# Performance work log

Measured on AMD Instinct MI355X. Metric: run time of the kernel, lower is better.

Reference implementation:

```python
import jax, jax.numpy as jnp
import numpy as np

EPS = 1e-8
B, T, D = 2, 512, 64
L = 4        # n_layers
NPASS = 2    # n_recursive_passes


def setup_inputs() -> dict:
    key = jax.random.key(0)
    ks = jax.random.split(key, 8)
    H = D // 2
    r = lambda k, shape, s=0.05: jax.random.normal(k, shape, dtype=jnp.float32) * s
    return {
        "basin_seq": jax.random.normal(ks[0], (B, T, D), dtype=jnp.float32),
        "basin_coords": r(ks[1], (D,), 0.1),
        "W_temp": r(ks[2], (L, 1, D)),
        "b_temp": jnp.zeros((L, 1), jnp.float32),
        "res_scale": jnp.full((L,), 0.1, jnp.float32),
        "W_fb": r(ks[3], (L, D, 2 * D)),
        "b_fb": jnp.zeros((L, D), jnp.float32),
        "Wc1": r(ks[4], (H, D)),
        "bc1": jnp.zeros((H,), jnp.float32),
        "Wc2": r(ks[5], (D, H)),
        "bc2": jnp.zeros((D,), jnp.float32),
        "Wu": r(ks[6], (D, 2 * D)),
        "bu": jnp.zeros((D,), jnp.float32),
        "res_scale_g": jnp.asarray(1.0, jnp.float32),
    }


def _project_to_simplex(x):
    s = jax.nn.softplus(x)
    s = s / (s.sum(axis=-1, keepdims=True) + EPS)
    return jnp.maximum(s, EPS)


def _qfi_attention_weights(x, temperature):
    # x: (B,T,D); temperature: scalar
    p = _project_to_simplex(x)
    # fisher_rao_distance_simplex renormalizes its inputs again
    p = p / (p.sum(axis=-1, keepdims=True) + EPS)
    # pairwise Bhattacharyya-like inner product: (B,T,T,D) broadcast -> (B,T,T)
    inner = jnp.sqrt(p[:, :, None, :] * p[:, None, :, :] + EPS).sum(axis=-1)
    inner = jnp.clip(inner, -1.0 + 1e-6, 1.0 - 1e-6)
    d = 2.0 * jnp.arccos(inner)                      # Fisher-Rao distance (B,T,T)
    logits = -d / jnp.maximum(temperature, 1e-6)
    return jax.nn.softmax(logits, axis=-1)


def _forward(basin_seq, basin_coords, W_temp, b_temp, res_scale, W_fb, b_fb,
             Wc1, bc1, Wc2, bc2, Wu, bu, res_scale_g):
    x = basin_seq
    current_basin = basin_coords                     # (D,)
    layer_states = [[None] * L for _ in range(NPASS)]
    for p_idx in range(NPASS):
        for l in range(L):
            prev = layer_states[p_idx - 1][l] if p_idx > 0 else None
            if prev is not None:
                combined = jnp.concatenate([x, prev], axis=-1)          # (B,T,2D)
                gate = jax.nn.sigmoid(combined @ W_fb[l].T + b_fb[l])   # (B,T,D)
                x = x * gate + prev * (1.0 - gate)
            # BasinCoupledQFIAttention (dropout inactive in eval)
            tm = jax.nn.sigmoid(W_temp[l] @ current_basin + b_temp[l]) + 0.5
            temperature = jax.lax.stop_gradient(tm.mean())  # torch uses .item()
            w = _qfi_attention_weights(x, temperature)
            x_attn = jnp.einsum('bij,bjd->bid', w, x)
            x = x + res_scale[l] * (x_attn - x)
            layer_states[p_idx][l] = x
        # holographic encode: mean-pool then compress MLP (tanh, tanh)
        pooled = x.mean(axis=1)                                         # (B,D)
        hidden_basin = jnp.tanh(jnp.tanh(pooled @ Wc1.T + bc1) @ Wc2.T + bc2)
        if p_idx < NPASS - 1:
            aggregated = hidden_basin.mean(axis=0)                      # (D,)
            comb = jnp.concatenate([current_basin, aggregated], axis=-1)
            g = jax.nn.sigmoid(Wu @ comb + bu)
            current_basin = current_basin * (1.0 - g) + aggregated * g
    output = x + 0.01 * res_scale_g * (x - basin_seq)
    return output


def reference(basin_seq, basin_coords, W_temp, b_temp, res_scale, W_fb, b_fb,
              Wc1, bc1, Wc2, bc2, Wu, bu, res_scale_g):
    return _forward(basin_seq, basin_coords, W_temp, b_temp, res_scale, W_fb,
                    b_fb, Wc1, bc1, Wc2, bc2, Wu, bu, res_scale_g)
```

## Files before the change

kernel.cpp:

```cpp
#include <hip/hip_runtime.h>
#include <math.h>

#define EPSF 1e-8f
#define Tn 512
#define Dn 64
#define NELEM 65536

typedef _Float16 half_t;
typedef __attribute__((ext_vector_type(4))) _Float16 half4;

__device__ __forceinline__ float sigmoidf_(float x){ return 1.0f/(1.0f+expf(-x)); }
__device__ __forceinline__ float softplusf_(float x){ return fmaxf(x,0.0f) + log1pf(expf(-fabsf(x))); }

__device__ __forceinline__ float wrs(float v){
  #pragma unroll
  for (int off=1; off<64; off<<=1) v += __shfl_xor(v, off, 64);
  return v;
}
__device__ __forceinline__ float wrm(float v){
  #pragma unroll
  for (int off=1; off<64; off<<=1) v = fmaxf(v, __shfl_xor(v, off, 64));
  return v;
}

__device__ __forceinline__ void pnorm_w(float xg, int b, int r, int row, int d,
                                        float* __restrict__ sbuf_out,
                                        half_t* __restrict__ sTh_out){
  float s = softplusf_(xg);
  float sum = wrs(s);
  float p = fmaxf(s/(sum+EPSF), EPSF);
  float s2 = wrs(p);
  float sq = sqrtf(p/(s2+EPSF));
  sbuf_out[(size_t)row*Dn + d] = sq;
  sTh_out[(size_t)b*Dn*Tn + (size_t)d*Tn + r] = (half_t)sq;
}

__global__ __launch_bounds__(256) void k_prologue(
    const float* __restrict__ basin_seq, float* __restrict__ sA, half_t* __restrict__ sThA,
    half_t* __restrict__ xhBS,
    const float* __restrict__ W_temp, const float* __restrict__ b_temp,
    const float* __restrict__ cb0, float* __restrict__ temps){
  int tid = threadIdx.x, wid = tid>>6, lane = tid&63;
  if (blockIdx.x < 256){
    int row = blockIdx.x*4 + wid;
    float xv = basin_seq[(size_t)row*Dn+lane];
    xhBS[(size_t)row*Dn+lane] = (half_t)xv;
    pnorm_w(xv, row>>9, row&511, row, lane, sA, sThA);
  } else if (tid < 64){
    float cbv = cb0[tid];
    #pragma unroll
    for (int l=0;l<4;l++){
      float v = wrs(W_temp[l*Dn + tid]*cbv);
      if (tid==0) temps[l] = sigmoidf_(v + b_temp[l]) + 0.5f;
    }
  }
}

__device__ __forceinline__ void gate_dot2(float (*comb)[128], float* gred,
                                          const float* __restrict__ Wfb, int tid, int lane){
  int dd = tid >> 3, k8 = tid & 7;
  const float4* wp = (const float4*)(Wfb + (size_t)dd*128 + k8*16);
  float4 w0 = wp[0], w1 = wp[1], w2 = wp[2], w3 = wp[3];
  float ga[2];
  #pragma unroll
  for (int i=0;i<2;i++){
    float4 c0 = *(const float4*)&comb[i][k8*16];
    float4 c1 = *(const float4*)&comb[i][k8*16+4];
    float4 c2 = *(const float4*)&comb[i][k8*16+8];
    float4 c3 = *(const float4*)&comb[i][k8*16+12];
    ga[i] = w0.x*c0.x + w0.y*c0.y + w0.z*c0.z + w0.w*c0.w
          + w1.x*c1.x + w1.y*c1.y + w1.z*c1.z + w1.w*c1.w
          + w2.x*c2.x + w2.y*c2.y + w2.z*c2.z + w2.w*c2.w
          + w3.x*c3.x + w3.y*c3.y + w3.z*c3.z + w3.w*c3.w;
  }
  #pragma unroll
  for (int off=1; off<8; off<<=1){
    ga[0] += __shfl_xor(ga[0],off,64); ga[1] += __shfl_xor(ga[1],off,64);
  }
  if ((lane&7)==0){ gred[dd*3+0]=ga[0]; gred[dd*3+1]=ga[1]; }
}

template<int MODE>
__global__ __launch_bounds__(512) void k_attn(
    const float* __restrict__ xin, const half_t* __restrict__ xh,
    const float* __restrict__ sbuf, const half_t* __restrict__ sTh,
    const float* __restrict__ temps, const float* __restrict__ res_scale, int l,
    float* __restrict__ xout, float* __restrict__ xg_out, half_t* __restrict__ xh_out,
    float* __restrict__ sbuf_out, half_t* __restrict__ sTh_out,
    const float* __restrict__ Wfb, const float* __restrict__ bfb,
    const float* __restrict__ prev,
    const float* __restrict__ basin_seq, const float* __restrict__ rsg,
    float* __restrict__ pooled_g, const float* __restrict__ basin_coords,
    const float* __restrict__ Wc1, const float* __restrict__ bc1,
    const float* __restrict__ Wc2, const float* __restrict__ bc2,
    const float* __restrict__ Wu,  const float* __restrict__ bu,
    const float* __restrict__ W_temp, const float* __restrict__ b_temp){
  __shared__ __align__(16) union {
    float part[8*512];
    float pvp[32*2*64];
  } u;
  __shared__ __align__(8) float P[512*2];
  __shared__ __align__(8) float s_i[64*2];
  __shared__ float redw[2][8][2];
  __shared__ __align__(16) float comb[2][128];
  __shared__ float gred[64*3];
  __shared__ float pl[128], h1b[64], hbb[128], combb[128];
  __shared__ float tl_sh;

  int tid = threadIdx.x, wav = tid>>6, lane = tid&63;
  int row0 = blockIdx.x*2, b = row0>>9, r0 = row0&511;
  int i_ = tid>>6, d_ = lane;

  float xi_pre = 0.f, prev_pre = 0.f;
  if (tid < 128){
    s_i[d_*2 + i_] = sbuf[(size_t)(row0+i_)*Dn + d_];
    xi_pre = xin[(size_t)(row0+i_)*Dn + d_];
    if constexpr (MODE == 4 || MODE == 5) prev_pre = prev[(size_t)(row0+i_)*Dn + d_];
  }

  if constexpr (MODE == 5 || MODE == 6){
    if (tid < 128) pl[tid] = pooled_g[tid] * (1.0f/512.0f);
    __syncthreads();
    if (tid < 64){
      int bb=tid>>5, h=tid&31;
      float acc=0.f;
      #pragma unroll 8
      for (int d2=0; d2<64; d2++) acc += pl[bb*64+d2]*Wc1[h*64+d2];
      h1b[tid] = tanhf(acc + bc1[h]);
    }
    __syncthreads();
    if (tid < 128){
      int bb=tid>>6, dd=tid&63;
      float acc=0.f;
      #pragma unroll 8
      for (int h2=0; h2<32; h2++) acc += h1b[bb*32+h2]*Wc2[dd*32+h2];
      hbb[tid] = tanhf(acc + bc2[dd]);
    }
    __syncthreads();
    if (tid < 64){
      float agg = 0.5f*(hbb[tid] + hbb[64+tid]);
      combb[tid] = basin_coords[tid];
      combb[64+tid] = agg;
    }
    __syncthreads();
    if (tid < 64){
      float acc=0.f;
      #pragma unroll 8
      for (int k=0;k<128;k++) acc += Wu[tid*128+k]*combb[k];
      float g = sigmoidf_(acc + bu[tid]);
      float cbl = combb[tid]*(1.0f-g) + combb[64+tid]*g;
      float v = wrs(W_temp[l*Dn + tid]*cbl);
      if (tid==0) tl_sh = sigmoidf_(v + b_temp[l]) + 0.5f;
    }
  }
  __syncthreads();

  {
    int g = tid & 127, kq = tid >> 7;
    const half4* sT4 = (const half4*)(sTh + (size_t)b*Dn*Tn);
    float4 a0 = {0,0,0,0}, a1 = a0;
    int kb = kq*16;
    #pragma unroll
    for (int kk=0; kk<16; ++kk){
      int k = kb + kk;
      half4 vh = sT4[(size_t)k*128 + g];
      float vx=(float)vh.x, vy=(float)vh.y, vz=(float)vh.z, vw=(float)vh.w;
      float2 si = *(const float2*)&s_i[k*2];
      a0.x=fmaf(si.x,vx,a0.x); a0.y=fmaf(si.x,vy,a0.y);
      a0.z=fmaf(si.x,vz,a0.z); a0.w=fmaf(si.x,vw,a0.w);
      a1.x=fmaf(si.y,vx,a1.x); a1.y=fmaf(si.y,vy,a1.y);
      a1.z=fmaf(si.y,vz,a1.z); a1.w=fmaf(si.y,vw,a1.w);
    }
    *(float4*)&u.part[(0*4+kq)*512 + g*4] = a0;
    *(float4*)&u.part[(1*4+kq)*512 + g*4] = a1;
  }
  __syncthreads();
  {
    float invT;
    if constexpr (MODE == 5 || MODE == 6) invT = 1.0f/fmaxf(tl_sh, 1e-6f);
    else invT = 1.0f/fmaxf(temps[l], 1e-6f);
    int j = tid;
    float a0 = u.part[0*512+j] + u.part[1*512+j] + u.part[2*512+j] + u.part[3*512+j];
    float a1 = u.part[4*512+j] + u.part[5*512+j] + u.part[6*512+j] + u.part[7*512+j];
    float l0 = -2.0f*acosf(fminf(fmaxf(a0,-1.0f+1e-6f),1.0f-1e-6f))*invT;
    float l1 = -2.0f*acosf(fminf(fmaxf(a1,-1.0f+1e-6f),1.0f-1e-6f))*invT;
    float m0=wrm(l0), m1=wrm(l1);
    if (lane==0){ redw[0][wav][0]=m0; redw[0][wav][1]=m1; }
    __syncthreads();
    float mv0=redw[0][0][0], mv1=redw[0][0][1];
    #pragma unroll
    for (int w=1;w<8;w++){ mv0=fmaxf(mv0,redw[0][w][0]); mv1=fmaxf(mv1,redw[0][w][1]); }
    float e0=expf(l0-mv0), e1=expf(l1-mv1);
    float2 ev = {e0,e1};
    *(float2*)&P[j*2] = ev;
    float q0=wrs(e0), q1=wrs(e1);
    if (lane==0){ redw[1][wav][0]=q0; redw[1][wav][1]=q1; }
  }
  __syncthreads();
  {
    int jg = tid>>4, dq = tid&15;
    const half4* x4 = (const half4*)(xh + (size_t)b*Tn*Dn);
    float4 o0={0,0,0,0}, o1=o0;
    int jb = jg*16;
    #pragma unroll
    for (int jj=0; jj<16; ++jj){
      int j = jb + jj;
      half4 xvh = x4[(size_t)j*16 + dq];
      float xx=(float)xvh.x, xy=(float)xvh.y, xz=(float)xvh.z, xw=(float)xvh.w;
      float2 pw = *(const float2*)&P[j*2];
      o0.x=fmaf(pw.x,xx,o0.x); o0.y=fmaf(pw.x,xy,o0.y);
      o0.z=fmaf(pw.x,xz,o0.z); o0.w=fmaf(pw.x,xw,o0.w);
      o1.x=fmaf(pw.y,xx,o1.x); o1.y=fmaf(pw.y,xy,o1.y);
      o1.z=fmaf(pw.y,xz,o1.z); o1.w=fmaf(pw.y,xw,o1.w);
    }
    *(float4*)&u.pvp[(jg*2+0)*64 + dq*4] = o0;
    *(float4*)&u.pvp[(jg*2+1)*64 + dq*4] = o1;
  }
  __syncthreads();
  float o = 0.f;
  if (tid < 128){
    float ss = 0.f;
    #pragma unroll
    for (int jg=0; jg<32; ++jg) ss += u.pvp[(jg*2+i_)*64+d_];
    float sv = 0.f;
    #pragma unroll
    for (int w=0;w<8;w++) sv += redw[1][w][i_];
    float attn = ss/sv;
    o = xi_pre + res_scale[l]*(attn - xi_pre);
  }
  if constexpr (MODE == 0){
    if (tid < 128){
      xout[(size_t)(row0+i_)*Dn + d_] = o;
      xh_out[(size_t)(row0+i_)*Dn + d_] = (half_t)o;
      pnorm_w(o, b, r0+i_, row0+i_, d_, sbuf_out, sTh_out);
    }
  } else if constexpr (MODE == 4){
    if (tid < 128){
      xout[(size_t)(row0+i_)*Dn + d_] = o;
      atomicAdd(&pooled_g[b*64+d_], o);
      comb[i_][d_] = o;
      comb[i_][64+d_] = prev_pre;
    }
    __syncthreads();
    gate_dot2(comb, gred, Wfb, tid, lane);
    __syncthreads();
    if (tid < 128){
      float g = sigmoidf_(gred[d_*3+i_] + bfb[d_]);
      float xg = o*g + prev_pre*(1.0f-g);
      xg_out[(size_t)(row0+i_)*Dn + d_] = xg;
      xh_out[(size_t)(row0+i_)*Dn + d_] = (half_t)xg;
      pnorm_w(xg, b, r0+i_, row0+i_, d_, sbuf_out, sTh_out);
    }
  } else if constexpr (MODE == 5){
    if (tid < 128){
      comb[i_][d_] = o;
      comb[i_][64+d_] = prev_pre;
    }
    __syncthreads();
    gate_dot2(comb, gred, Wfb, tid, lane);
    __syncthreads();
    if (tid < 128){
      float g = sigmoidf_(gred[d_*3+i_] + bfb[d_]);
      float xg = o*g + prev_pre*(1.0f-g);
      xout[(size_t)(row0+i_)*Dn + d_] = xg;
      xh_out[(size_t)(row0+i_)*Dn + d_] = (half_t)xg;
      pnorm_w(xg, b, r0+i_, row0+i_, d_, sbuf_out, sTh_out);
    }
  } else {
    if (tid < 128){
      float c = 0.01f * rsg[0];
      xout[(size_t)(row0+i_)*Dn + d_] = o + c*(o - basin_seq[(size_t)(row0+i_)*Dn + d_]);
    }
  }
}

extern "C" void kernel_launch(void* const* d_in, const int* in_sizes, int n_in,
                              void* d_out, int out_size, void* d_ws, size_t ws_size,
                              hipStream_t stream) {
  const float* basin_seq    = (const float*)d_in[0];
  const float* basin_coords = (const float*)d_in[1];
  const float* W_temp       = (const float*)d_in[2];
  const float* b_temp       = (const float*)d_in[3];
  const float* res_scale    = (const float*)d_in[4];
  const float* W_fb         = (const float*)d_in[5];
  const float* b_fb         = (const float*)d_in[6];
  const float* Wc1          = (const float*)d_in[7];
  const float* bc1          = (const float*)d_in[8];
  const float* Wc2          = (const float*)d_in[9];
  const float* bc2          = (const float*)d_in[10];
  const float* Wu           = (const float*)d_in[11];
  const float* bu           = (const float*)d_in[12];
  const float* rsg          = (const float*)d_in[13];
  float* out = (float*)d_out;
  float* ws  = (float*)d_ws;

  const size_t N = NELEM;
  float* pooled_g = ws;
  float* temps    = ws + 192;
  float* base     = ws + 256;
  float* sA    = base;
  float* sB    = base + N;
  float* st0   = base + 2*N;
  float* st1   = base + 3*N;
  float* st2   = base + 4*N;
  float* st3   = base + 5*N;
  float* xA    = base + 6*N;
  float* xB    = base + 7*N;
  half_t* sThA = (half_t*)(base + 8*N);
  half_t* sThB = (half_t*)(base + 8*N + N/2);
  half_t* xhBS = (half_t*)(base + 9*N);
  half_t* xhA  = (half_t*)(base + 9*N + N/2);
  half_t* xhB  = (half_t*)(base + 10*N);

  const int GA = 512;

  (void)hipMemsetAsync(d_ws, 0, 1024, stream);

  k_prologue<<<257,256,0,stream>>>(basin_seq, sA, sThA, xhBS, W_temp, b_temp, basin_coords, temps);
  k_attn<0><<<GA,512,0,stream>>>(basin_seq, xhBS, sA, sThA, temps, res_scale, 0,
                                 st0, nullptr, xhA, sB, sThB,
                                 nullptr,nullptr,nullptr,nullptr,nullptr,
                                 nullptr,nullptr,nullptr,nullptr,nullptr,nullptr,nullptr,nullptr,nullptr,nullptr);
  k_attn<0><<<GA,512,0,stream>>>(st0, xhA, sB, sThB, temps, res_scale, 1,
                                 st1, nullptr, xhB, sA, sThA,
                                 nullptr,nullptr,nullptr,nullptr,nullptr,
                                 nullptr,nullptr,nullptr,nullptr,nullptr,nullptr,nullptr,nullptr,nullptr,nullptr);
  k_attn<0><<<GA,512,0,stream>>>(st1, xhB, sA, sThA, temps, res_scale, 2,
                                 st2, nullptr, xhA, sB, sThB,
                                 nullptr,nullptr,nullptr,nullptr,nullptr,
                                 nullptr,nullptr,nullptr,nullptr,nullptr,nullptr,nullptr,nullptr,nullptr,nullptr);
  k_attn<4><<<GA,512,0,stream>>>(st2, xhA, sB, sThB, temps, res_scale, 3,
                                 st3, xA, xhBS, sA, sThA,
                                 W_fb, b_fb, st0, nullptr,nullptr,
                                 pooled_g,nullptr,nullptr,nullptr,nullptr,nullptr,nullptr,nullptr,nullptr,nullptr);
  k_attn<5><<<GA,512,0,stream>>>(xA, xhBS, sA, sThA, nullptr, res_scale, 0,
                                 xB, nullptr, xhA, sB, sThB,
                                 W_fb + (size_t)1*Dn*2*Dn, b_fb + 1*Dn, st1, nullptr,nullptr,
                                 pooled_g, basin_coords, Wc1, bc1, Wc2, bc2, Wu, bu, W_temp, b_temp);
  k_attn<5><<<GA,512,0,stream>>>(xB, xhA, sB, sThB, nullptr, res_scale, 1,
                                 xA, nullptr, xhB, sA, sThA,
                                 W_fb + (size_t)2*Dn*2*Dn, b_fb + 2*Dn, st2, nullptr,nullptr,
                                 pooled_g, basin_coords, Wc1, bc1, Wc2, bc2, Wu, bu, W_temp, b_temp);
  k_attn<5><<<GA,512,0,stream>>>(xA, xhB, sA, sThA, nullptr, res_scale, 2,
                                 xB, nullptr, xhA, sB, sThB,
                                 W_fb + (size_t)3*Dn*2*Dn, b_fb + 3*Dn, st3, nullptr,nullptr,
                                 pooled_g, basin_coords, Wc1, bc1, Wc2, bc2, Wu, bu, W_temp, b_temp);
  k_attn<6><<<GA,512,0,stream>>>(xB, xhA, sB, sThB, nullptr, res_scale, 3,
                                 out, nullptr, nullptr, nullptr, nullptr,
                                 nullptr,nullptr,nullptr, basin_seq, rsg,
                                 pooled_g, basin_coords, Wc1, bc1, Wc2, bc2, Wu, bu, W_temp, b_temp);
}
```

Baseline: 199.1 us.

## Compute pass-two temperatures once in last block via atomic counter

Before, every block of the four second-pass attention kernels recomputed the compress MLP, the basin update and the temperature from pooled_g, each step separated by block barriers. Now the last block to finish the MODE 4 kernel, found through a threadfence and an atomic counter, computes all four second-pass temperatures once and writes them to a workspace array. Later kernels just read temps[l]. This removes redundant serial prologue work from four launches per block, at the cost of a grid-wide atomic and a serial tail in a single block.

```diff
diff --git a/kernel.cpp b/kernel.cpp
--- a/kernel.cpp
+++ b/kernel.cpp
@@ -90,7 +90,8 @@
     const float* __restrict__ Wfb, const float* __restrict__ bfb,
     const float* __restrict__ prev,
     const float* __restrict__ basin_seq, const float* __restrict__ rsg,
-    float* __restrict__ pooled_g, const float* __restrict__ basin_coords,
+    float* __restrict__ pooled_g, unsigned* __restrict__ cnt,
+    float* __restrict__ temps_out, const float* __restrict__ basin_coords,
     const float* __restrict__ Wc1, const float* __restrict__ bc1,
     const float* __restrict__ Wc2, const float* __restrict__ bc2,
     const float* __restrict__ Wu,  const float* __restrict__ bu,
@@ -105,7 +106,7 @@
   __shared__ __align__(16) float comb[2][128];
   __shared__ float gred[64*3];
   __shared__ float pl[128], h1b[64], hbb[128], combb[128];
-  __shared__ float tl_sh;
+  __shared__ bool lastf;
 
   int tid = threadIdx.x, wav = tid>>6, lane = tid&63;
   int row0 = blockIdx.x*2, b = row0>>9, r0 = row0&511;
@@ -115,46 +116,11 @@
   if (tid < 128){
     s_i[d_*2 + i_] = sbuf[(size_t)(row0+i_)*Dn + d_];
     xi_pre = xin[(size_t)(row0+i_)*Dn + d_];
-    if constexpr (MODE == 4 || MODE == 5) prev_pre = prev[(size_t)(row0+i_)*Dn + d_];
-  }
-
-  if constexpr (MODE == 5 || MODE == 6){
-    if (tid < 128) pl[tid] = pooled_g[tid] * (1.0f/512.0f);
-    __syncthreads();
-    if (tid < 64){
-      int bb=tid>>5, h=tid&31;
-      float acc=0.f;
-      #pragma unroll 8
-      for (int d2=0; d2<64; d2++) acc += pl[bb*64+d2]*Wc1[h*64+d2];
-      h1b[tid] = tanhf(acc + bc1[h]);
-    }
-    __syncthreads();
-    if (tid < 128){
-      int bb=tid>>6, dd=tid&63;
-      float acc=0.f;
-      #pragma unroll 8
-      for (int h2=0; h2<32; h2++) acc += h1b[bb*32+h2]*Wc2[dd*32+h2];
-      hbb[tid] = tanhf(acc + bc2[dd]);
-    }
-    __syncthreads();
-    if (tid < 64){
-      float agg = 0.5f*(hbb[tid] + hbb[64+tid]);
-      combb[tid] = basin_coords[tid];
-      combb[64+tid] = agg;
-    }
-    __syncthreads();
-    if (tid < 64){
-      float acc=0.f;
-      #pragma unroll 8
-      for (int k=0;k<128;k++) acc += Wu[tid*128+k]*combb[k];
-      float g = sigmoidf_(acc + bu[tid]);
-      float cbl = combb[tid]*(1.0f-g) + combb[64+tid]*g;
-      float v = wrs(W_temp[l*Dn + tid]*cbl);
-      if (tid==0) tl_sh = sigmoidf_(v + b_temp[l]) + 0.5f;
-    }
+    if constexpr (MODE == 4 || MODE == 2) prev_pre = prev[(size_t)(row0+i_)*Dn + d_];
   }
   __syncthreads();
 
+  float invT = 1.0f/fmaxf(temps[l], 1e-6f);
   {
     int g = tid & 127, kq = tid >> 7;
     const half4* sT4 = (const half4*)(sTh + (size_t)b*Dn*Tn);
@@ -176,9 +142,6 @@
   }
   __syncthreads();
   {
-    float invT;
-    if constexpr (MODE == 5 || MODE == 6) invT = 1.0f/fmaxf(tl_sh, 1e-6f);
-    else invT = 1.0f/fmaxf(temps[l], 1e-6f);
     int j = tid;
     float a0 = u.part[0*512+j] + u.part[1*512+j] + u.part[2*512+j] + u.part[3*512+j];
     float a1 = u.part[4*512+j] + u.part[5*512+j] + u.part[6*512+j] + u.part[7*512+j];
@@ -251,7 +214,53 @@
       xh_out[(size_t)(row0+i_)*Dn + d_] = (half_t)xg;
       pnorm_w(xg, b, r0+i_, row0+i_, d_, sbuf_out, sTh_out);
     }
-  } else if constexpr (MODE == 5){
+    __syncthreads();
+    if (tid == 0){
+      __threadfence();
+      unsigned old = atomicAdd(cnt, 1u);
+      lastf = (old == gridDim.x - 1);
+    }
+    __syncthreads();
+    if (lastf){
+      if (tid < 128)
+        pl[tid] = __hip_atomic_load(&pooled_g[tid], __ATOMIC_RELAXED, __HIP_MEMORY_SCOPE_AGENT) * (1.0f/512.0f);
+      __syncthreads();
+      if (tid < 64){
+        int bb=tid>>5, h=tid&31;
+        float acc=0.f;
+        #pragma unroll 8
+        for (int d2=0; d2<64; d2++) acc += pl[bb*64+d2]*Wc1[h*64+d2];
+        h1b[tid] = tanhf(acc + bc1[h]);
+      }
+      __syncthreads();
+      if (tid < 128){
+        int bb=tid>>6, dd=tid&63;
+        float acc=0.f;
+        #pragma unroll 8
+        for (int h2=0; h2<32; h2++) acc += h1b[bb*32+h2]*Wc2[dd*32+h2];
+        hbb[tid] = tanhf(acc + bc2[dd]);
+      }
+      __syncthreads();
+      if (tid < 64){
+        float agg = 0.5f*(hbb[tid] + hbb[64+tid]);
+        combb[tid] = basin_coords[tid];
+        combb[64+tid] = agg;
+      }
+      __syncthreads();
+      if (tid < 64){
+        float acc=0.f;
+        #pragma unroll 8
+        for (int k=0;k<128;k++) acc += Wu[tid*128+k]*combb[k];
+        float g = sigmoidf_(acc + bu[tid]);
+        float cbl = combb[tid]*(1.0f-g) + combb[64+tid]*g;
+        #pragma unroll
+        for (int ll=0; ll<4; ll++){
+          float v = wrs(W_temp[ll*Dn + tid]*cbl);
+          if (tid==0) temps_out[ll] = sigmoidf_(v + b_temp[ll]) + 0.5f;
+        }
+      }
+    }
+  } else if constexpr (MODE == 2){
     if (tid < 128){
       comb[i_][d_] = o;
       comb[i_][64+d_] = prev_pre;
@@ -296,7 +305,9 @@
 
   const size_t N = NELEM;
   float* pooled_g = ws;
-  float* temps    = ws + 192;
+  unsigned* cnt   = (unsigned*)(ws + 160);
+  float* temps0   = ws + 192;
+  float* temps1   = ws + 224;
   float* base     = ws + 256;
   float* sA    = base;
   float* sB    = base + N;
@@ -316,37 +327,38 @@
 
   (void)hipMemsetAsync(d_ws, 0, 1024, stream);
 
-  k_prologue<<<257,256,0,stream>>>(basin_seq, sA, sThA, xhBS, W_temp, b_temp, basin_coords, temps);
-  k_attn<0><<<GA,512,0,stream>>>(basin_seq, xhBS, sA, sThA, temps, res_scale, 0,
+  k_prologue<<<257,256,0,stream>>>(basin_seq, sA, sThA, xhBS, W_temp, b_temp, basin_coords, temps0);
+  k_attn<0><<<GA,512,0,stream>>>(basin_seq, xhBS, sA, sThA, temps0, res_scale, 0,
                                  st0, nullptr, xhA, sB, sThB,
                                  nullptr,nullptr,nullptr,nullptr,nullptr,
-                                 nullptr,nullptr,nullptr,nullptr,nullptr,nullptr,nullptr,nullptr,nullptr,nullptr);
-  k_attn<0><<<GA,512,0,stream>>>(st0, xhA, sB, sThB, temps, res_scale, 1,
+                                 nullptr,nullptr,nullptr,nullptr,nullptr,nullptr,nullptr,nullptr,nullptr,nullptr,nullptr,nullptr);
+  k_attn<0><<<GA,512,0,stream>>>(st0, xhA, sB, sThB, temps0, res_scale, 1,
                                  st1, nullptr, xhB, sA, sThA,
                                  nullptr,nullptr,nullptr,nullptr,nullptr,
-                                 nullptr,nullptr,nullptr,nullptr,nullptr,nullptr,nullptr,nullptr,nullptr,nullptr);
-  k_attn<0><<<GA,512,0,stream>>>(st1, xhB, sA, sThA, temps, res_scale, 2,
+                                 nullptr,nullptr,nullptr,nullptr,nullptr,nullptr,nullptr,nullptr,nullptr,nullptr,nullptr,nullptr);
+  k_attn<0><<<GA,512,0,stream>>>(st1, xhB, sA, sThA, temps0, res_scale, 2,
                                  st2, nullptr, xhA, sB, sThB,
                                  nullptr,nullptr,nullptr,nullptr,nullptr,
-                                 nullptr,nullptr,nullptr,nullptr,nullptr,nullptr,nullptr,nullptr,nullptr,nullptr);
-  k_attn<4><<<GA,512,0,stream>>>(st2, xhA, sB, sThB, temps, res_scale, 3,
+                                 nullptr,nullptr,nullptr,nullptr,nullptr,nullptr,nullptr,nullptr,nullptr,nullptr,nullptr,nullptr);
+  k_attn<4><<<GA,512,0,stream>>>(st2, xhA, sB, sThB, temps0, res_scale, 3,
                                  st3, xA, xhBS, sA, sThA,
                                  W_fb, b_fb, st0, nullptr,nullptr,
-                                 pooled_g,nullptr,nullptr,nullptr,nullptr,nullptr,nullptr,nullptr,nullptr,nullptr);
-  k_attn<5><<<GA,512,0,stream>>>(xA, xhBS, sA, sThA, nullptr, res_scale, 0,
+                                 pooled_g, cnt, temps1, basin_coords,
+                                 Wc1, bc1, Wc2, bc2, Wu, bu, W_temp, b_temp);
+  k_attn<2><<<GA,512,0,stream>>>(xA, xhBS, sA, sThA, temps1, res_scale, 0,
                                  xB, nullptr, xhA, sB, sThB,
                                  W_fb + (size_t)1*Dn*2*Dn, b_fb + 1*Dn, st1, nullptr,nullptr,
-                                 pooled_g, basin_coords, Wc1, bc1, Wc2, bc2, Wu, bu, W_temp, b_temp);
-  k_attn<5><<<GA,512,0,stream>>>(xB, xhA, sB, sThB, nullptr, res_scale, 1,
+                                 nullptr,nullptr,nullptr,nullptr,nullptr,nullptr,nullptr,nullptr,nullptr,nullptr,nullptr,nullptr);
+  k_attn<2><<<GA,512,0,stream>>>(xB, xhA, sB, sThB, temps1, res_scale, 1,
                                  xA, nullptr, xhB, sA, sThA,
                                  W_fb + (size_t)2*Dn*2*Dn, b_fb + 2*Dn, st2, nullptr,nullptr,
-                                 pooled_g, basin_coords, Wc1, bc1, Wc2, bc2, Wu, bu, W_temp, b_temp);
-  k_attn<5><<<GA,512,0,stream>>>(xA, xhB, sA, sThA, nullptr, res_scale, 2,
+                                 nullptr,nullptr,nullptr,nullptr,nullptr,nullptr,nullptr,nullptr,nullptr,nullptr,nullptr,nullptr);
+  k_attn<2><<<GA,512,0,stream>>>(xA, xhB, sA, sThA, temps1, res_scale, 2,
                                  xB, nullptr, xhA, sB, sThB,
                                  W_fb + (size_t)3*Dn*2*Dn, b_fb + 3*Dn, st3, nullptr,nullptr,
-                                 pooled_g, basin_coords, Wc1, bc1, Wc2, bc2, Wu, bu, W_temp, b_temp);
-  k_attn<6><<<GA,512,0,stream>>>(xB, xhA, sB, sThB, nullptr, res_scale, 3,
+                                 nullptr,nullptr,nullptr,nullptr,nullptr,nullptr,nullptr,nullptr,nullptr,nullptr,nullptr,nullptr);
+  k_attn<3><<<GA,512,0,stream>>>(xB, xhA, sB, sThB, temps1, res_scale, 3,
                                  out, nullptr, nullptr, nullptr, nullptr,
                                  nullptr,nullptr,nullptr, basin_seq, rsg,
-                                 pooled_g, basin_coords, Wc1, bc1, Wc2, bc2, Wu, bu, W_temp, b_temp);
-}
+                                 nullptr,nullptr,nullptr,nullptr,nullptr,nullptr,nullptr,nullptr,nullptr,nullptr,nullptr,nullptr);
+}
```

Result: no change. 196.1 us (-1.5%).
